# Performance work log

Measured on AMD Instinct MI355X. Metric: run time of the kernel, lower is better.

The kernel has to match this reference:

```python
import jax, jax.numpy as jnp
import numpy as np
from jax import lax

HEADS = 8
DIM_HEAD = 8
SCALE = DIM_HEAD ** (-0.5)
UP = 64  # nn.Upsample(scale_factor=64), nearest


def _conv_s8(x, w, b):
    # Conv2d(inner, inner, 11x11, stride 8, padding 2) + exact GELU
    y = lax.conv_general_dilated(x, w, window_strides=(8, 8),
                                 padding=((2, 2), (2, 2)),
                                 dimension_numbers=('NCHW', 'OIHW', 'NCHW'))
    return jax.nn.gelu(y + b[None, :, None, None], approximate=False)


def setup_inputs() -> dict:
    key = jax.random.key(0)
    ks = jax.random.split(key, 8)
    b, c, h, w = 2, 64, 48, 48
    inner = HEADS * DIM_HEAD  # 64
    f = jax.random.normal(ks[0], (b, c, h, w), jnp.float32)
    w_qkv = jax.random.normal(ks[1], (inner * 3, c, 1, 1), jnp.float32) * 0.05
    wq = jax.random.normal(ks[2], (inner, inner, 11, 11), jnp.float32) * 0.02
    bq = jax.random.normal(ks[3], (inner,), jnp.float32) * 0.02
    wk = jax.random.normal(ks[4], (inner, inner, 11, 11), jnp.float32) * 0.02
    bk = jax.random.normal(ks[5], (inner,), jnp.float32) * 0.02
    pos_h = jax.random.normal(ks[6], (DIM_HEAD, h), jnp.float32) * SCALE
    pos_w = jax.random.normal(ks[7], (DIM_HEAD, w), jnp.float32) * SCALE
    return {"f": f, "w_qkv": w_qkv, "wq": wq, "bq": bq, "wk": wk,
            "bk": bk, "pos_h": pos_h, "pos_w": pos_w}


def reference(f, w_qkv, wq, bq, wk, bk, pos_h, pos_w):
    b, c, h, w = f.shape
    inner = HEADS * DIM_HEAD
    # 1x1 conv to qkv
    qkv = jnp.einsum('oc,bchw->bohw', w_qkv[:, :, 0, 0], f)
    q, k, v = jnp.split(qkv, 3, axis=1)  # each [b, inner, h, w]
    # positional logits from pre-conv q
    q_full = q.reshape(b, HEADS, DIM_HEAD, h * w)
    emb = (pos_h[:, :, None] + pos_w[:, None, :]).reshape(DIM_HEAD, h * w)
    pos_logits = jnp.einsum('bhci,cj->bhij', q_full, emb)  # [b,H,hw,hw]
    # strided conv + gelu on q,k
    qd = _conv_s8(q, wq, bq)
    kd = _conv_s8(k, wk, bk)
    m = qd.shape[-1]  # downsampled side
    qd = qd.reshape(b, HEADS, DIM_HEAD, m * m) * SCALE
    kd = kd.reshape(b, HEADS, DIM_HEAD, m * m)
    vv = v.reshape(b, HEADS, DIM_HEAD, h * w)
    dots = jnp.einsum('bhci,bhcj->bhij', qd, kd)  # [b,H,m^2,m^2]
    # nearest upsample x64 on last two dims
    dots = jnp.repeat(jnp.repeat(dots, UP, axis=-2), UP, axis=-1)
    attn = jax.nn.softmax(dots + pos_logits, axis=-1)
    fmap = jnp.einsum('bhij,bhcj->bhci', attn, vv)
    return fmap.reshape(b, inner, h, w)
```

## Files before the change

### kernel.cpp

```cpp
#include <hip/hip_runtime.h>
#include <math.h>

#define HW 2304
#define O192 192
#define SCALE_F 0.35355339059327373f

typedef unsigned int u32;
typedef __attribute__((address_space(1))) const u32 gu32;
typedef __attribute__((address_space(3))) u32 lu32;
__device__ __forceinline__ void dma16(const void* g, void* l) {
  __builtin_amdgcn_global_load_lds((gu32*)g, (lu32*)l, 16, 0, 0);
}

__global__ __launch_bounds__(256) void qkv_kernel(
    const float* __restrict__ F, const float* __restrict__ W,
    float* __restrict__ QKV, float* __restrict__ V2) {
  __shared__ __align__(16) float sW[384];
  int blk = blockIdx.x;
  int idx0 = blk * 256;
  int r0 = idx0 / HW;
  int r1 = (idx0 + 255) / HW;
  int tid = threadIdx.x;
  if (tid < 192) {
    int g = tid >> 6, c = tid & 63;
    sW[tid]       = W[((r0 & 63) + g * 64) * 64 + c];
    sW[192 + tid] = W[((r1 & 63) + g * 64) * 64 + c];
  }
  __syncthreads();
  int idx = idx0 + tid;
  int p  = idx % HW;
  int r  = idx / HW;
  int o0 = r & 63;
  int b  = r >> 6;
  const float4* w4 = (const float4*)(sW + ((r == r0) ? 0 : 192));
  const float* f = F + (b * 64) * HW + p;
  float aq = 0.f, ak = 0.f, av = 0.f;
  #pragma unroll 4
  for (int c4 = 0; c4 < 16; c4++) {
    float4 wq = w4[c4];
    float4 wk = w4[16 + c4];
    float4 wv = w4[32 + c4];
    float f0 = f[(c4 * 4 + 0) * HW];
    float f1 = f[(c4 * 4 + 1) * HW];
    float f2 = f[(c4 * 4 + 2) * HW];
    float f3 = f[(c4 * 4 + 3) * HW];
    aq = fmaf(wq.x, f0, aq); ak = fmaf(wk.x, f0, ak); av = fmaf(wv.x, f0, av);
    aq = fmaf(wq.y, f1, aq); ak = fmaf(wk.y, f1, ak); av = fmaf(wv.y, f1, av);
    aq = fmaf(wq.z, f2, aq); ak = fmaf(wk.z, f2, ak); av = fmaf(wv.z, f2, av);
    aq = fmaf(wq.w, f3, aq); ak = fmaf(wk.w, f3, ak); av = fmaf(wv.w, f3, av);
  }
  float* qp = QKV + (b * HW + p) * O192;
  qp[o0]      = aq;
  qp[o0 + 64] = ak;
  V2[(((b << 3) + (o0 >> 3)) * HW + p) * 8 + (o0 & 7)] = av;
}

__global__ __launch_bounds__(256) void conv_kernel(
    const float* __restrict__ QKV, const float* __restrict__ Wq,
    const float* __restrict__ Bq, const float* __restrict__ Wk,
    const float* __restrict__ Bk, float* __restrict__ QD) {
  __shared__ float sW[7744];
  __shared__ float sRed[4 * 64 * 6];
  int blk = blockIdx.x;
  int xcd = blk & 7;
  int T = xcd >> 2, b = (xcd >> 1) & 1, s = xcd & 1;
  int idx = (blk >> 3) * 2 + s;
  int o  = idx / 6;
  int oy = idx % 6;
  const float* Wg = T ? Wk : Wq;
  for (int i = threadIdx.x; i < 7744; i += 256) sW[i] = Wg[o * 7744 + i];
  __syncthreads();
  int wv = threadIdx.x >> 6;
  int c  = threadIdx.x & 63;
  const float* base = QKV + b * (HW * O192) + T * 64 + c;
  float acc[6];
  #pragma unroll
  for (int ox = 0; ox < 6; ox++) acc[ox] = 0.f;
  for (int kyi = 0; kyi < 3; kyi++) {
    int ky = wv * 3 + kyi;
    if (ky > 10) break;
    int y = oy * 8 - 2 + ky;
    if ((unsigned)y < 48u) {
      float xrow[48];
      #pragma unroll
      for (int x = 0; x < 48; x++) xrow[x] = base[(y * 48 + x) * O192];
      #pragma unroll
      for (int kx = 0; kx < 11; kx++) {
        float wt = sW[c * 121 + ky * 11 + kx];
        #pragma unroll
        for (int ox = 0; ox < 6; ox++) {
          int x = ox * 8 - 2 + kx;
          if (x >= 0 && x < 48) acc[ox] = fmaf(xrow[x], wt, acc[ox]);
        }
      }
    }
  }
  #pragma unroll
  for (int ox = 0; ox < 6; ox++) sRed[(wv * 64 + c) * 6 + ox] = acc[ox];
  __syncthreads();
  if (threadIdx.x < 64) {
    int t = threadIdx.x;
    float r[6];
    #pragma unroll
    for (int ox = 0; ox < 6; ox++)
      r[ox] = sRed[t * 6 + ox] + sRed[(64 + t) * 6 + ox]
            + sRed[(128 + t) * 6 + ox] + sRed[(192 + t) * 6 + ox];
    #pragma unroll
    for (int off = 32; off; off >>= 1) {
      #pragma unroll
      for (int ox = 0; ox < 6; ox++) r[ox] += __shfl_down(r[ox], off, 64);
    }
    if (t == 0) {
      float bias = T ? Bk[o] : Bq[o];
      #pragma unroll
      for (int ox = 0; ox < 6; ox++) {
        float g = r[ox] + bias;
        float ge = 0.5f * g * (1.0f + erff(g * 0.70710678118654752f));
        QD[((T * 2 + b) * 64 + o) * 36 + oy * 6 + ox] = ge;
      }
    }
  }
}

__global__ __launch_bounds__(256) void dots_kernel(
    const float* __restrict__ QD, float* __restrict__ E) {
  int idx = blockIdx.x * 256 + threadIdx.x;
  if (idx >= 16 * 36 * 36) return;
  int J  = idx % 36;
  int I  = (idx / 36) % 36;
  int bh = idx / 1296;
  int b = bh >> 3, h = bh & 7;
  float acc = 0.f;
  #pragma unroll
  for (int c8 = 0; c8 < 8; c8++) {
    float qv = QD[((0 + b) * 64 + h * 8 + c8) * 36 + I];
    float kv = QD[((2 + b) * 64 + h * 8 + c8) * 36 + J];
    acc = fmaf(qv, kv, acc);
  }
  E[idx] = __expf(SCALE_F * acc);
}

#define OFF_V   0
#define OFF_EA  4608
#define OFF_PHT 7680
#define OFF_PWT 8064
#define OFF_E4  8448
#define OFF_U   8592
#define SBUF_N  13200

__global__ __launch_bounds__(512, 4) void attn_kernel(
    const float* __restrict__ QKV, const float* __restrict__ V2,
    const float* __restrict__ E, const float* __restrict__ PH,
    const float* __restrict__ PW, float* __restrict__ Pnum,
    float* __restrict__ PZ) {
  __shared__ __align__(16) float sB[SBUF_N];
  int blk = blockIdx.x;
  int bh = blk / 36;
  int rem = blk - bh * 36;
  int q = rem & 3, S = rem >> 2;
  int b = bh >> 3, h = bh & 7;
  int tid = threadIdx.x;
  int w = tid >> 6, lane = tid & 63;
  if (tid < 384) {
    sB[OFF_PHT + tid] = PH[(tid & 7) * 48 + (tid >> 3)];
    sB[OFF_PWT + tid] = PW[(tid & 7) * 48 + (tid >> 3)];
  }
  if (tid < 144) {
    int J = tid >> 2, k = tid & 3;
    sB[OFF_E4 + tid] = E[bh * 1296 + (S * 4 + k) * 36 + J];
  }
  {
    int row = tid >> 1, half = tid & 1;
    *(float4*)(sB + OFF_U + tid * 4) =
      *(const float4*)(QKV + (b * HW + S * 256 + row) * O192 + h * 8 + half * 4);
  }
  {
    const char* src = (const char*)(V2 + (size_t)bh * (HW * 8) + q * 4608);
    for (int m = w; m < 18; m += 8)
      dma16(src + m * 1024 + lane * 16, (char*)(sB + OFF_V) + m * 1024);
  }
  __syncthreads();
  #pragma unroll
  for (int m = 0; m < 6; m++) {
    int flat = tid + m * 512;
    int jyL = flat >> 8, rl = flat & 255;
    int ln = rl >> 2, kk = rl & 3;
    const float* qp = sB + OFF_U + (kk * 64 + ln) * 8;
    const float* pp = sB + OFF_PHT + (q * 12 + jyL) * 8;
    float d = qp[0]*pp[0]+qp[1]*pp[1]+qp[2]*pp[2]+qp[3]*pp[3]
            + qp[4]*pp[4]+qp[5]*pp[5]+qp[6]*pp[6]+qp[7]*pp[7];
    sB[OFF_EA + flat] = __expf(d);
  }
  float eB[4][6];
  #pragma unroll
  for (int k = 0; k < 4; k++) {
    const float* qp = sB + OFF_U + (k * 64 + lane) * 8;
    #pragma unroll
    for (int i = 0; i < 6; i++) {
      const float* pp = sB + OFF_PWT + (w * 6 + i) * 8;
      float d = qp[0]*pp[0]+qp[1]*pp[1]+qp[2]*pp[2]+qp[3]*pp[3]
              + qp[4]*pp[4]+qp[5]*pp[5]+qp[6]*pp[6]+qp[7]*pp[7];
      eB[k][i] = __expf(d);
    }
  }
  __syncthreads();
  float acc[4][9];
  #pragma unroll
  for (int k = 0; k < 4; k++)
    #pragma unroll
    for (int c = 0; c < 9; c++) acc[k][c] = 0.f;
  const float4* sV4 = (const float4*)(sB + OFF_V);
  for (int jyL = 0; jyL < 12; jyL++) {
    float4 eAk = *(const float4*)(sB + OFF_EA + jyL * 256 + lane * 4);
    int cb = (q * 12 + jyL) * 48 + w * 6;
    int J0 = cb >> 6, J1 = (cb + 5) >> 6;
    int ib = 64 - (cb & 63);
    float4 e0 = *(const float4*)(sB + OFF_E4 + J0 * 4);
    float4 e1 = *(const float4*)(sB + OFF_E4 + J1 * 4);
    float a0[4] = {eAk.x*e0.x, eAk.y*e0.y, eAk.z*e0.z, eAk.w*e0.w};
    float a1[4] = {eAk.x*e1.x, eAk.y*e1.y, eAk.z*e1.z, eAk.w*e1.w};
    #pragma unroll
    for (int i = 0; i < 6; i++) {
      float4 vlo = sV4[(jyL * 48 + w * 6 + i) * 2];
      float4 vhi = sV4[(jyL * 48 + w * 6 + i) * 2 + 1];
      bool sel = (i < ib);
      #pragma unroll
      for (int k = 0; k < 4; k++) {
        float wgt = (sel ? a0[k] : a1[k]) * eB[k][i];
        acc[k][0] = fmaf(wgt, vlo.x, acc[k][0]);
        acc[k][1] = fmaf(wgt, vlo.y, acc[k][1]);
        acc[k][2] = fmaf(wgt, vlo.z, acc[k][2]);
        acc[k][3] = fmaf(wgt, vlo.w, acc[k][3]);
        acc[k][4] = fmaf(wgt, vhi.x, acc[k][4]);
        acc[k][5] = fmaf(wgt, vhi.y, acc[k][5]);
        acc[k][6] = fmaf(wgt, vhi.z, acc[k][6]);
        acc[k][7] = fmaf(wgt, vhi.w, acc[k][7]);
        acc[k][8] += wgt;
      }
    }
  }
  float* sU = sB + OFF_U;
  #pragma unroll
  for (int k = 0; k < 4; k++) {
    #pragma unroll
    for (int c = 0; c < 9; c++) sU[(w * 64 + lane) * 9 + c] = acc[k][c];
    __syncthreads();
    {
      int c = tid >> 6, r = tid & 63;
      float num = 0.f;
      #pragma unroll
      for (int ww = 0; ww < 8; ww++) num += sU[(ww * 64 + r) * 9 + c];
      Pnum[((q * 16 + bh) * 8 + c) * HW + S * 256 + k * 64 + r] = num;
      if (tid < 64) {
        float z = 0.f;
        #pragma unroll
        for (int ww = 0; ww < 8; ww++) z += sU[(ww * 64 + tid) * 9 + 8];
        PZ[(q * 16 + bh) * HW + S * 256 + k * 64 + tid] = z;
      }
    }
    __syncthreads();
  }
}

__global__ __launch_bounds__(256) void combine_kernel(
    const float* __restrict__ Pnum, const float* __restrict__ PZ,
    float* __restrict__ out) {
  int t = blockIdx.x * 256 + threadIdx.x;
  int row = t % HW;
  int rc = t / HW;
  int c = rc & 7, bh = rc >> 3;
  float num = 0.f, z = 0.f;
  #pragma unroll
  for (int q = 0; q < 4; q++) {
    num += Pnum[((q * 16 + bh) * 8 + c) * HW + row];
    z   += PZ[(q * 16 + bh) * HW + row];
  }
  int b = bh >> 3, h = bh & 7;
  out[(b * 64 + h * 8 + c) * HW + row] = num / z;
}

extern "C" void kernel_launch(void* const* d_in, const int* in_sizes, int n_in,
                              void* d_out, int out_size, void* d_ws, size_t ws_size,
                              hipStream_t stream) {
  const float* F    = (const float*)d_in[0];
  const float* Wqkv = (const float*)d_in[1];
  const float* Wq   = (const float*)d_in[2];
  const float* Bq   = (const float*)d_in[3];
  const float* Wk   = (const float*)d_in[4];
  const float* Bk   = (const float*)d_in[5];
  const float* PH   = (const float*)d_in[6];
  const float* PW   = (const float*)d_in[7];
  float* out = (float*)d_out;

  float* ws   = (float*)d_ws;
  float* QKV  = ws;
  float* V2   = QKV + 2 * HW * O192;
  float* QD   = V2 + 2 * 8 * HW * 8;
  float* E    = QD + 2 * 2 * 64 * 36;
  float* Pnum = E + 16 * 36 * 36;
  float* PZ   = Pnum + 4 * 16 * 8 * HW;

  qkv_kernel    <<<1152, 256, 0, stream>>>(F, Wqkv, QKV, V2);
  conv_kernel   <<<1536, 256, 0, stream>>>(QKV, Wq, Bq, Wk, Bk, QD);
  dots_kernel   <<<81,   256, 0, stream>>>(QD, E);
  attn_kernel   <<<576,  512, 0, stream>>>(QKV, V2, E, PH, PW, Pnum, PZ);
  combine_kernel<<<1152, 256, 0, stream>>>(Pnum, PZ, out);
}
```

Baseline: 142.1 us.

## Fuse dots into attention and replace combine kernel with last-block reduction

Removes the separate dots kernel by computing the 36-element exp(q·k) slice directly inside each attention block from QD. Removes the combine kernel by having each attention block bump an atomic counter per (bh, S) tile, so the last of the four q-splits reduces Pnum/PZ and writes the normalized output. Cuts two kernel launches and the E buffer round trip, at the cost of an atomic, thread fences and a serialized tail reduction in the final blocks. The counters are zeroed by the qkv kernel.

```diff
diff --git a/kernel.cpp b/kernel.cpp
--- a/kernel.cpp
+++ b/kernel.cpp
@@ -14,13 +14,14 @@
 
 __global__ __launch_bounds__(256) void qkv_kernel(
     const float* __restrict__ F, const float* __restrict__ W,
-    float* __restrict__ QKV, float* __restrict__ V2) {
+    float* __restrict__ QKV, float* __restrict__ V2, u32* __restrict__ Cnt) {
   __shared__ __align__(16) float sW[384];
   int blk = blockIdx.x;
   int idx0 = blk * 256;
   int r0 = idx0 / HW;
   int r1 = (idx0 + 255) / HW;
   int tid = threadIdx.x;
+  if (blk == 0 && tid < 144) Cnt[tid] = 0;
   if (tid < 192) {
     int g = tid >> 6, c = tid & 63;
     sW[tid]       = W[((r0 & 63) + g * 64) * 64 + c];
@@ -122,24 +123,6 @@
   }
 }
 
-__global__ __launch_bounds__(256) void dots_kernel(
-    const float* __restrict__ QD, float* __restrict__ E) {
-  int idx = blockIdx.x * 256 + threadIdx.x;
-  if (idx >= 16 * 36 * 36) return;
-  int J  = idx % 36;
-  int I  = (idx / 36) % 36;
-  int bh = idx / 1296;
-  int b = bh >> 3, h = bh & 7;
-  float acc = 0.f;
-  #pragma unroll
-  for (int c8 = 0; c8 < 8; c8++) {
-    float qv = QD[((0 + b) * 64 + h * 8 + c8) * 36 + I];
-    float kv = QD[((2 + b) * 64 + h * 8 + c8) * 36 + J];
-    acc = fmaf(qv, kv, acc);
-  }
-  E[idx] = __expf(SCALE_F * acc);
-}
-
 #define OFF_V   0
 #define OFF_EA  4608
 #define OFF_PHT 7680
@@ -150,10 +133,11 @@
 
 __global__ __launch_bounds__(512, 4) void attn_kernel(
     const float* __restrict__ QKV, const float* __restrict__ V2,
-    const float* __restrict__ E, const float* __restrict__ PH,
+    const float* __restrict__ QD, const float* __restrict__ PH,
     const float* __restrict__ PW, float* __restrict__ Pnum,
-    float* __restrict__ PZ) {
+    float* __restrict__ PZ, u32* __restrict__ Cnt, float* __restrict__ out) {
   __shared__ __align__(16) float sB[SBUF_N];
+  __shared__ int sLast;
   int blk = blockIdx.x;
   int bh = blk / 36;
   int rem = blk - bh * 36;
@@ -167,7 +151,14 @@
   }
   if (tid < 144) {
     int J = tid >> 2, k = tid & 3;
-    sB[OFF_E4 + tid] = E[bh * 1296 + (S * 4 + k) * 36 + J];
+    float acc = 0.f;
+    #pragma unroll
+    for (int c8 = 0; c8 < 8; c8++) {
+      float qv = QD[((0 + b) * 64 + h * 8 + c8) * 36 + (S * 4 + k)];
+      float kv = QD[((2 + b) * 64 + h * 8 + c8) * 36 + J];
+      acc = fmaf(qv, kv, acc);
+    }
+    sB[OFF_E4 + tid] = __expf(SCALE_F * acc);
   }
   {
     int row = tid >> 1, half = tid & 1;
@@ -260,23 +251,30 @@
     }
     __syncthreads();
   }
-}
-
-__global__ __launch_bounds__(256) void combine_kernel(
-    const float* __restrict__ Pnum, const float* __restrict__ PZ,
-    float* __restrict__ out) {
-  int t = blockIdx.x * 256 + threadIdx.x;
-  int row = t % HW;
-  int rc = t / HW;
-  int c = rc & 7, bh = rc >> 3;
-  float num = 0.f, z = 0.f;
-  #pragma unroll
-  for (int q = 0; q < 4; q++) {
-    num += Pnum[((q * 16 + bh) * 8 + c) * HW + row];
-    z   += PZ[(q * 16 + bh) * HW + row];
-  }
-  int b = bh >> 3, h = bh & 7;
-  out[(b * 64 + h * 8 + c) * HW + row] = num / z;
+  __threadfence();
+  __syncthreads();
+  if (tid == 0) {
+    u32 old = atomicAdd(&Cnt[bh * 9 + S], 1u);
+    sLast = (old == 3u);
+  }
+  __syncthreads();
+  if (sLast) {
+    __threadfence();
+    int r = tid & 255, cg = tid >> 8;
+    float z = 0.f;
+    #pragma unroll
+    for (int qq = 0; qq < 4; qq++)
+      z += PZ[(qq * 16 + bh) * HW + S * 256 + r];
+    #pragma unroll
+    for (int cc = 0; cc < 4; cc++) {
+      int c = cg * 4 + cc;
+      float num = 0.f;
+      #pragma unroll
+      for (int qq = 0; qq < 4; qq++)
+        num += Pnum[((qq * 16 + bh) * 8 + c) * HW + S * 256 + r];
+      out[(b * 64 + h * 8 + c) * HW + S * 256 + r] = num / z;
+    }
+  }
 }
 
 extern "C" void kernel_launch(void* const* d_in, const int* in_sizes, int n_in,
@@ -296,13 +294,11 @@
   float* QKV  = ws;
   float* V2   = QKV + 2 * HW * O192;
   float* QD   = V2 + 2 * 8 * HW * 8;
-  float* E    = QD + 2 * 2 * 64 * 36;
-  float* Pnum = E + 16 * 36 * 36;
+  float* Pnum = QD + 2 * 2 * 64 * 36;
   float* PZ   = Pnum + 4 * 16 * 8 * HW;
-
-  qkv_kernel    <<<1152, 256, 0, stream>>>(F, Wqkv, QKV, V2);
-  conv_kernel   <<<1536, 256, 0, stream>>>(QKV, Wq, Bq, Wk, Bk, QD);
-  dots_kernel   <<<81,   256, 0, stream>>>(QD, E);
-  attn_kernel   <<<576,  512, 0, stream>>>(QKV, V2, E, PH, PW, Pnum, PZ);
-  combine_kernel<<<1152, 256, 0, stream>>>(Pnum, PZ, out);
-}
+  u32*   Cnt  = (u32*)(PZ + 4 * 16 * HW);
+
+  qkv_kernel <<<1152, 256, 0, stream>>>(F, Wqkv, QKV, V2, Cnt);
+  conv_kernel<<<1536, 256, 0, stream>>>(QKV, Wq, Bq, Wk, Bk, QD);
+  attn_kernel<<<576,  512, 0, stream>>>(QKV, V2, QD, PH, PW, Pnum, PZ, Cnt, out);
+}
```

Result: slower. 253.1 us (+78.1%).
